# Kernel optimization log

Measured on AMD Instinct MI355X. Metric: run time of the kernel, lower is better.

Reference implementation:

```python
import jax, jax.numpy as jnp
import numpy as np

OUTPUT_SIZE = 16384          # number of map units (must be a perfect square)
SIDE = 128.0                 # sqrt(OUTPUT_SIZE)
SIGMA = 2.0                  # neighbourhood std-dev (non-trainable weight in original)
B, D = 2048, 256


def setup_inputs() -> dict:
    key = jax.random.key(0)
    k1, k2 = jax.random.split(key)
    x = jax.random.normal(k1, (B, D), dtype=jnp.float32)
    kernel = jax.random.normal(k2, (D, OUTPUT_SIZE), dtype=jnp.float32) * 0.1
    return {"x": x, "kernel": kernel}


def _grid_coords():
    # 2D coordinates of each flattened map unit: unit k -> (k // side, k % side)
    idx = jnp.arange(OUTPUT_SIZE, dtype=jnp.float32)
    return jnp.floor(idx / SIDE), jnp.mod(idx, SIDE)  # each (size,)


def reference(x, kernel):
    # Squared Euclidean distance of every sample to every prototype: (B, size).
    # Same math as tf.norm(x[:, :, None] - kernel[None])**2, expressed as a GEMM.
    norms2 = (jnp.sum(x * x, axis=1, keepdims=True)
              - 2.0 * (x @ kernel)
              + jnp.sum(kernel * kernel, axis=0, keepdims=True))
    norms2 = jnp.maximum(norms2, 0.0)

    # Winner-take-all unit per sample, mapped to 2D grid coordinates.
    wta = jnp.argmin(norms2, axis=1).astype(jnp.float32)        # (B,)
    mean_r = jnp.floor(wta / SIDE)                               # (B,)
    mean_c = jnp.mod(wta, SIDE)                                  # (B,)

    # Gaussian neighbourhood over the 2D grid, flattened: (B, size).
    gr, gc = _grid_coords()
    dr = gr[None, :] - mean_r[:, None]
    dc = gc[None, :] - mean_c[:, None]
    radials = jnp.exp(-0.5 / (SIGMA * SIGMA) * (dr * dr + dc * dc))

    return radials * norms2
```

## Files before the change

kernel.cpp:

```cpp
#include <hip/hip_runtime.h>
#include <hip/hip_fp16.h>

#define OUTN 16384
#define BATCH 2048
#define DIM   256

typedef _Float16 half8 __attribute__((ext_vector_type(8)));
typedef float    floatx4 __attribute__((ext_vector_type(4)));
typedef unsigned long long u64;

__device__ __forceinline__ void gl2lds16(const void* g, void* l) {
    __builtin_amdgcn_global_load_lds(
        (const __attribute__((address_space(1))) void*)g,
        (__attribute__((address_space(3))) void*)l, 16, 0, 0);
}

__device__ __forceinline__ u64 packkey(float v, int col) {
    unsigned u = __float_as_uint(v);
    u = (u & 0x80000000u) ? ~u : (u | 0x80000000u);
    return ((u64)u << 32) | (unsigned)col;
}
__device__ __forceinline__ float unpackval(u64 p) {
    unsigned u = (unsigned)(p >> 32);
    u = (u & 0x80000000u) ? (u & 0x7fffffffu) : ~u;
    return __uint_as_float(u);
}

__global__ __launch_bounds__(256) void prep_all(
        const float* __restrict__ x, const float* __restrict__ kern,
        _Float16* __restrict__ xh, float* __restrict__ rown,
        _Float16* __restrict__ kT, float* __restrict__ colnp) {
    int blk = blockIdx.x, t = threadIdx.x;
    if (blk < 512) {
        __shared__ float tile[64][65];
        __shared__ float npart[4][64];
        int tx = t & 63, ty = t >> 6;
        int j0 = (blk >> 1) * 64;
        int dhalf = blk & 1, dbase = dhalf * 128;
        float nrm = 0.f;
        for (int pc = 0; pc < 2; pc++) {
            int dc = dbase + pc * 64;
            __syncthreads();
            for (int it = 0; it < 16; it++) {
                int d = dc + ty + it * 4;
                float v = kern[(size_t)d * OUTN + j0 + tx];
                tile[ty + it * 4][tx] = v;
                nrm = fmaf(v, v, nrm);
            }
            __syncthreads();
            for (int c = t; c < 512; c += 256) {
                int j = c >> 3, o8 = (c & 7) * 8;
                half8 h;
                for (int u = 0; u < 8; u++) h[u] = (_Float16)tile[o8 + u][j];
                *(half8*)&kT[(size_t)(j0 + j) * DIM + dc + o8] = h;
            }
        }
        npart[ty][tx] = nrm;
        __syncthreads();
        if (t < 64)
            colnp[(size_t)dhalf * OUTN + j0 + t] =
                npart[0][t] + npart[1][t] + npart[2][t] + npart[3][t];
    } else {
        int b = blk - 512;
        float v = x[b * DIM + t];
        xh[b * DIM + t] = (_Float16)v;
        float s = v * v;
        for (int off = 32; off; off >>= 1) s += __shfl_down(s, off, 64);
        __shared__ float wsum[4];
        if ((t & 63) == 0) wsum[t >> 6] = s;
        __syncthreads();
        if (t == 0) rown[b] = wsum[0] + wsum[1] + wsum[2] + wsum[3];
    }
}

template <bool NF16>
__global__ __launch_bounds__(256) void gemm_norms(
        const _Float16* __restrict__ xh, const _Float16* __restrict__ kT,
        const float* __restrict__ rown, const float* __restrict__ colnp,
        void* __restrict__ n2out, u64* __restrict__ blockcand) {
    __shared__ __align__(16) char smem[32768];
    _Float16* As = (_Float16*)smem;
    _Float16* Bs = (_Float16*)(smem + 16384);
    u64* cand = (u64*)smem;
    int tid  = threadIdx.x;
    int col0 = blockIdx.x * 128;
    int row0 = blockIdx.y * 128;
    int wid = tid >> 6, lane = tid & 63;
    int wr = wid >> 1, wc = wid & 1;
    int l15 = lane & 15, l4 = lane >> 4;
    int xh7 = l15 & 7;

    floatx4 acc[4][4];
    for (int i = 0; i < 4; i++)
        for (int j = 0; j < 4; j++)
            acc[i][j] = (floatx4){0.f, 0.f, 0.f, 0.f};

    for (int kt = 0; kt < 4; kt++) {
        int k0 = kt * 64;
        for (int it = 0; it < 4; it++) {
            int chunk = it * 256 + tid;
            int r = chunk >> 3, gg = chunk & 7;
            int ksw = (gg ^ (r & 7)) * 8;
            gl2lds16(&xh[(size_t)(row0 + r) * DIM + k0 + ksw], &As[chunk * 8]);
            gl2lds16(&kT[(size_t)(col0 + r) * DIM + k0 + ksw], &Bs[chunk * 8]);
        }
        __syncthreads();
        for (int s = 0; s < 2; s++) {
            int g = s * 4 + l4;
            int sw = (g ^ xh7) * 8;
            half8 af[4], bf[4];
            for (int i = 0; i < 4; i++)
                af[i] = *(half8*)&As[(wr * 64 + i * 16 + l15) * 64 + sw];
            for (int j = 0; j < 4; j++)
                bf[j] = *(half8*)&Bs[(wc * 64 + j * 16 + l15) * 64 + sw];
            for (int i = 0; i < 4; i++)
                for (int j = 0; j < 4; j++)
                    acc[i][j] = __builtin_amdgcn_mfma_f32_16x16x32_f16(
                        af[i], bf[j], acc[i][j], 0, 0, 0);
        }
        __syncthreads();
    }

    float cn[4]; int oc[4];
    for (int j = 0; j < 4; j++) {
        oc[j] = col0 + wc * 64 + j * 16 + l15;
        cn[j] = colnp[oc[j]] + colnp[OUTN + oc[j]];
    }
    for (int i = 0; i < 4; i++) {
        for (int r = 0; r < 4; r++) {
            int row_l = wr * 64 + i * 16 + l4 * 4 + r;
            int orow  = row0 + row_l;
            float rn = rown[orow];
            u64 best = ~0ull;
            for (int j = 0; j < 4; j++) {
                float val = rn + cn[j] - 2.0f * acc[i][j][r];
                size_t oi = (size_t)orow * OUTN + oc[j];
                if (NF16) ((_Float16*)n2out)[oi] = (_Float16)val;
                else      ((float*)n2out)[oi]    = val;
                u64 p = packkey(val, oc[j]);
                if (p < best) best = p;
            }
            cand[row_l * 32 + wc * 16 + l15] = best;
        }
    }
    __syncthreads();
    if (tid < 128) {
        u64 m1 = ~0ull, m2 = ~0ull;
        for (int s = 0; s < 32; s++) {
            u64 v = cand[tid * 32 + s];
            if (v < m1) { m2 = m1; m1 = v; }
            else if (v < m2) { m2 = v; }
        }
        size_t base = (size_t)(row0 + tid) * 256 + blockIdx.x * 2;
        blockcand[base]     = m1;
        blockcand[base + 1] = m2;
    }
}

template <bool NF16>
__global__ __launch_bounds__(256) void refine_finalize(
        const u64* __restrict__ blockcand, const float* __restrict__ x,
        const float* __restrict__ kern, const float* __restrict__ colnp,
        const void* __restrict__ n2in, float* __restrict__ out) {
    int b = blockIdx.x, t = threadIdx.x;
    __shared__ float xrow[DIM];
    __shared__ u64 red[256];
    xrow[t] = x[b * DIM + t];
    u64 e = blockcand[(size_t)b * 256 + t];
    red[t] = e;
    __syncthreads();
    for (int off = 128; off; off >>= 1) {
        if (t < off) { u64 o = red[t + off]; if (o < red[t]) red[t] = o; }
        __syncthreads();
    }
    float minv = unpackval(red[0]);
    __syncthreads();

    float ve = unpackval(e);
    u64 p = ~0ull;
    if (ve <= minv + 0.125f) {
        int j = (int)(e & 0xffffffffu);
        float dot = 0.f;
        for (int d = 0; d < DIM; d++)
            dot = fmaf(xrow[d], kern[(size_t)d * OUTN + j], dot);
        p = packkey((colnp[j] + colnp[OUTN + j]) - 2.0f * dot, j);
    }
    red[t] = p;
    __syncthreads();
    for (int off = 128; off; off >>= 1) {
        if (t < off) { u64 o = red[t + off]; if (o < red[t]) red[t] = o; }
        __syncthreads();
    }
    int w = (int)(red[0] & 0xffffffffu);
    int wrr = w >> 7, wcc = w & 127;

    const _Float16* r16 = (const _Float16*)n2in + (size_t)b * OUTN;
    const float*    r32 = (const float*)n2in    + (size_t)b * OUTN;
    float* rowp = out + (size_t)b * OUTN;
    for (int it = 0; it < 16; it++) {
        int idx4 = it * 256 + t;
        int j0 = idx4 * 4;
        int r  = j0 >> 7, c0 = j0 & 127;
        int dr = r - wrr, drsq = dr * dr;
        float4 res;
        {
            int dc = c0 - wcc;     int d2 = drsq + dc * dc;
            float v = (d2 <= 720) ? (NF16 ? (float)r16[j0]     : r32[j0])     : 0.f;
            res.x = (d2 <= 720) ? __expf(-0.125f * (float)d2) * fmaxf(v, 0.f) : 0.f;
        }
        {
            int dc = c0 + 1 - wcc; int d2 = drsq + dc * dc;
            float v = (d2 <= 720) ? (NF16 ? (float)r16[j0 + 1] : r32[j0 + 1]) : 0.f;
            res.y = (d2 <= 720) ? __expf(-0.125f * (float)d2) * fmaxf(v, 0.f) : 0.f;
        }
        {
            int dc = c0 + 2 - wcc; int d2 = drsq + dc * dc;
            float v = (d2 <= 720) ? (NF16 ? (float)r16[j0 + 2] : r32[j0 + 2]) : 0.f;
            res.z = (d2 <= 720) ? __expf(-0.125f * (float)d2) * fmaxf(v, 0.f) : 0.f;
        }
        {
            int dc = c0 + 3 - wcc; int d2 = drsq + dc * dc;
            float v = (d2 <= 720) ? (NF16 ? (float)r16[j0 + 3] : r32[j0 + 3]) : 0.f;
            res.w = (d2 <= 720) ? __expf(-0.125f * (float)d2) * fmaxf(v, 0.f) : 0.f;
        }
        ((float4*)rowp)[idx4] = res;
    }
}

extern "C" void kernel_launch(void* const* d_in, const int* in_sizes, int n_in,
                              void* d_out, int out_size, void* d_ws, size_t ws_size,
                              hipStream_t stream) {
    const float* x    = (const float*)d_in[0];
    const float* kern = (const float*)d_in[1];
    float* out = (float*)d_out;
    char* ws = (char*)d_ws;

    _Float16* xh   = (_Float16*)(ws);
    _Float16* kT   = (_Float16*)(ws + (1u << 20));
    float*   colnp = (float*)(ws + (9u << 20));
    float*   rown  = (float*)(ws + (9u << 20) + (128u << 10));
    u64* blockcand = (u64*)(ws + (10u << 20));
    void*    n2h   = (void*)(ws + (14u << 20));
    bool f16path = ws_size >= ((size_t)78 << 20);

    prep_all<<<2560, 256, 0, stream>>>(x, kern, xh, rown, kT, colnp);
    if (f16path) {
        gemm_norms<true><<<dim3(OUTN / 128, BATCH / 128), 256, 0, stream>>>(
            xh, kT, rown, colnp, n2h, blockcand);
        refine_finalize<true><<<BATCH, 256, 0, stream>>>(
            blockcand, x, kern, colnp, n2h, out);
    } else {
        gemm_norms<false><<<dim3(OUTN / 128, BATCH / 128), 256, 0, stream>>>(
            xh, kT, rown, colnp, (void*)out, blockcand);
        refine_finalize<false><<<BATCH, 256, 0, stream>>>(
            blockcand, x, kern, colnp, (const void*)out, out);
    }
}
```

Measured before the change: 202.1 us.

## Fuse all stages into one persistent kernel with grid barriers

Replaces the three launches with a single persistent 512-block kernel that uses software grid barriers between the prep, GEMM+candidate, refine and finalize phases. It also adds an fp32 transposed kernel copy so the refine dot product reads contiguously, and stages the fp16 norms tile in LDS for coalesced writes. Finalize now uses separable precomputed Gaussian row/column factors and skips rows beyond the cutoff. The change targets launch overhead and uncoalesced accesses, but it depends on all 512 blocks being co-resident for the spin barrier, drops the fp32 fallback path, and each block serializes four column tiles of GEMM work.

Measured after the change: 502.6 us. 2.49x slower.

```diff
diff --git a/kernel.cpp b/kernel.cpp
--- a/kernel.cpp
+++ b/kernel.cpp
@@ -4,6 +4,7 @@
 #define OUTN 16384
 #define BATCH 2048
 #define DIM   256
+#define NBLK  512
 
 typedef _Float16 half8 __attribute__((ext_vector_type(8)));
 typedef float    floatx4 __attribute__((ext_vector_type(4)));
@@ -26,17 +27,33 @@
     return __uint_as_float(u);
 }
 
-__global__ __launch_bounds__(256) void prep_all(
+__device__ __forceinline__ void gridbar(unsigned* bar, unsigned target) {
+    __syncthreads();
+    __threadfence();
+    if (threadIdx.x == 0) {
+        atomicAdd(bar, 1u);
+        while (atomicAdd(bar, 0u) < target) __builtin_amdgcn_s_sleep(2);
+    }
+    __syncthreads();
+    __threadfence();
+}
+
+__global__ __launch_bounds__(256, 2) void som_fused(
         const float* __restrict__ x, const float* __restrict__ kern,
-        _Float16* __restrict__ xh, float* __restrict__ rown,
-        _Float16* __restrict__ kT, float* __restrict__ colnp) {
-    int blk = blockIdx.x, t = threadIdx.x;
-    if (blk < 512) {
-        __shared__ float tile[64][65];
-        __shared__ float npart[4][64];
+        _Float16* __restrict__ xh, _Float16* __restrict__ kT,
+        float* __restrict__ kT32, float* __restrict__ colnp,
+        float* __restrict__ rown, u64* __restrict__ blockcand,
+        int* __restrict__ wta, _Float16* __restrict__ n2h,
+        float* __restrict__ out, unsigned* __restrict__ bar) {
+    __shared__ __align__(16) char smem[34816];
+    int p = blockIdx.x, t = threadIdx.x;
+
+    {
+        float (*tile)[65] = (float(*)[65])smem;
+        float* npart = (float*)(smem + 16640);
         int tx = t & 63, ty = t >> 6;
-        int j0 = (blk >> 1) * 64;
-        int dhalf = blk & 1, dbase = dhalf * 128;
+        int j0 = (p >> 1) * 64;
+        int dhalf = p & 1, dbase = dhalf * 128;
         float nrm = 0.f;
         for (int pc = 0; pc < 2; pc++) {
             int dc = dbase + pc * 64;
@@ -50,180 +67,194 @@
             __syncthreads();
             for (int c = t; c < 512; c += 256) {
                 int j = c >> 3, o8 = (c & 7) * 8;
-                half8 h;
-                for (int u = 0; u < 8; u++) h[u] = (_Float16)tile[o8 + u][j];
+                half8 h; float vv[8];
+                for (int u = 0; u < 8; u++) { vv[u] = tile[o8 + u][j]; h[u] = (_Float16)vv[u]; }
                 *(half8*)&kT[(size_t)(j0 + j) * DIM + dc + o8] = h;
-            }
-        }
-        npart[ty][tx] = nrm;
+                float* kp = &kT32[(size_t)(j0 + j) * DIM + dc + o8];
+                *(float4*)kp       = make_float4(vv[0], vv[1], vv[2], vv[3]);
+                *(float4*)(kp + 4) = make_float4(vv[4], vv[5], vv[6], vv[7]);
+            }
+        }
+        npart[ty * 64 + tx] = nrm;
         __syncthreads();
         if (t < 64)
             colnp[(size_t)dhalf * OUTN + j0 + t] =
-                npart[0][t] + npart[1][t] + npart[2][t] + npart[3][t];
-    } else {
-        int b = blk - 512;
-        float v = x[b * DIM + t];
-        xh[b * DIM + t] = (_Float16)v;
-        float s = v * v;
-        for (int off = 32; off; off >>= 1) s += __shfl_down(s, off, 64);
-        __shared__ float wsum[4];
-        if ((t & 63) == 0) wsum[t >> 6] = s;
+                npart[t] + npart[64 + t] + npart[128 + t] + npart[192 + t];
         __syncthreads();
-        if (t == 0) rown[b] = wsum[0] + wsum[1] + wsum[2] + wsum[3];
-    }
-}
-
-template <bool NF16>
-__global__ __launch_bounds__(256) void gemm_norms(
-        const _Float16* __restrict__ xh, const _Float16* __restrict__ kT,
-        const float* __restrict__ rown, const float* __restrict__ colnp,
-        void* __restrict__ n2out, u64* __restrict__ blockcand) {
-    __shared__ __align__(16) char smem[32768];
-    _Float16* As = (_Float16*)smem;
-    _Float16* Bs = (_Float16*)(smem + 16384);
-    u64* cand = (u64*)smem;
-    int tid  = threadIdx.x;
-    int col0 = blockIdx.x * 128;
-    int row0 = blockIdx.y * 128;
-    int wid = tid >> 6, lane = tid & 63;
-    int wr = wid >> 1, wc = wid & 1;
-    int l15 = lane & 15, l4 = lane >> 4;
-    int xh7 = l15 & 7;
-
-    floatx4 acc[4][4];
-    for (int i = 0; i < 4; i++)
-        for (int j = 0; j < 4; j++)
-            acc[i][j] = (floatx4){0.f, 0.f, 0.f, 0.f};
-
-    for (int kt = 0; kt < 4; kt++) {
-        int k0 = kt * 64;
-        for (int it = 0; it < 4; it++) {
-            int chunk = it * 256 + tid;
-            int r = chunk >> 3, gg = chunk & 7;
-            int ksw = (gg ^ (r & 7)) * 8;
-            gl2lds16(&xh[(size_t)(row0 + r) * DIM + k0 + ksw], &As[chunk * 8]);
-            gl2lds16(&kT[(size_t)(col0 + r) * DIM + k0 + ksw], &Bs[chunk * 8]);
-        }
-        __syncthreads();
-        for (int s = 0; s < 2; s++) {
-            int g = s * 4 + l4;
-            int sw = (g ^ xh7) * 8;
-            half8 af[4], bf[4];
-            for (int i = 0; i < 4; i++)
-                af[i] = *(half8*)&As[(wr * 64 + i * 16 + l15) * 64 + sw];
-            for (int j = 0; j < 4; j++)
-                bf[j] = *(half8*)&Bs[(wc * 64 + j * 16 + l15) * 64 + sw];
+        for (int q = 0; q < 4; q++) {
+            int b = p * 4 + q;
+            float v = x[b * DIM + t];
+            xh[b * DIM + t] = (_Float16)v;
+            float s = v * v;
+            for (int off = 32; off; off >>= 1) s += __shfl_down(s, off, 64);
+            if ((t & 63) == 0) npart[t >> 6] = s;
+            __syncthreads();
+            if (t == 0) rown[b] = npart[0] + npart[1] + npart[2] + npart[3];
+            __syncthreads();
+        }
+    }
+    gridbar(bar, NBLK);
+
+    {
+        int rb = p >> 5, cg = p & 31;
+        int row0 = rb * 128;
+        int wid = t >> 6, lane = t & 63;
+        int wr = wid >> 1, wc = wid & 1;
+        int l15 = lane & 15, l4 = lane >> 4;
+        int xh7 = l15 & 7;
+        _Float16* As = (_Float16*)smem;
+        _Float16* Bs = (_Float16*)(smem + 16384);
+        u64* cand = (u64*)smem;
+        _Float16* nb = (_Float16*)smem;
+
+        for (int cc = 0; cc < 4; cc++) {
+            int cb = cg * 4 + cc;
+            int col0 = cb * 128;
+            floatx4 acc[4][4];
             for (int i = 0; i < 4; i++)
                 for (int j = 0; j < 4; j++)
-                    acc[i][j] = __builtin_amdgcn_mfma_f32_16x16x32_f16(
-                        af[i], bf[j], acc[i][j], 0, 0, 0);
-        }
+                    acc[i][j] = (floatx4){0.f, 0.f, 0.f, 0.f};
+
+            for (int kt = 0; kt < 4; kt++) {
+                int k0 = kt * 64;
+                for (int it = 0; it < 4; it++) {
+                    int chunk = it * 256 + t;
+                    int r = chunk >> 3, gg = chunk & 7;
+                    int ksw = (gg ^ (r & 7)) * 8;
+                    gl2lds16(&xh[(size_t)(row0 + r) * DIM + k0 + ksw], &As[chunk * 8]);
+                    gl2lds16(&kT[(size_t)(col0 + r) * DIM + k0 + ksw], &Bs[chunk * 8]);
+                }
+                __syncthreads();
+                for (int s = 0; s < 2; s++) {
+                    int g = s * 4 + l4;
+                    int sw = (g ^ xh7) * 8;
+                    half8 af[4], bf[4];
+                    for (int i = 0; i < 4; i++)
+                        af[i] = *(half8*)&As[(wr * 64 + i * 16 + l15) * 64 + sw];
+                    for (int j = 0; j < 4; j++)
+                        bf[j] = *(half8*)&Bs[(wc * 64 + j * 16 + l15) * 64 + sw];
+                    for (int i = 0; i < 4; i++)
+                        for (int j = 0; j < 4; j++)
+                            acc[i][j] = __builtin_amdgcn_mfma_f32_16x16x32_f16(
+                                af[i], bf[j], acc[i][j], 0, 0, 0);
+                }
+                __syncthreads();
+            }
+
+            float cn[4]; int oc[4];
+            for (int j = 0; j < 4; j++) {
+                oc[j] = col0 + wc * 64 + j * 16 + l15;
+                cn[j] = colnp[oc[j]] + colnp[OUTN + oc[j]];
+            }
+            for (int i = 0; i < 4; i++) {
+                for (int r = 0; r < 4; r++) {
+                    int row_l = wr * 64 + i * 16 + l4 * 4 + r;
+                    u64 best = ~0ull;
+                    for (int j = 0; j < 4; j++) {
+                        u64 pk = packkey(cn[j] - 2.0f * acc[i][j][r], oc[j]);
+                        if (pk < best) best = pk;
+                    }
+                    cand[row_l * 33 + wc * 16 + l15] = best;
+                }
+            }
+            __syncthreads();
+            if (t < 128) {
+                u64 m1 = ~0ull, m2 = ~0ull;
+                for (int s = 0; s < 32; s++) {
+                    u64 v = cand[t * 33 + s];
+                    if (v < m1) { m2 = m1; m1 = v; }
+                    else if (v < m2) { m2 = v; }
+                }
+                size_t base = (size_t)(row0 + t) * 256 + cb * 2;
+                blockcand[base]     = m1;
+                blockcand[base + 1] = m2;
+            }
+            __syncthreads();
+            for (int i = 0; i < 4; i++) {
+                for (int r = 0; r < 4; r++) {
+                    int row_l = wr * 64 + i * 16 + l4 * 4 + r;
+                    float rn = rown[row0 + row_l];
+                    for (int j = 0; j < 4; j++)
+                        nb[row_l * 128 + wc * 64 + j * 16 + l15] =
+                            (_Float16)(rn + cn[j] - 2.0f * acc[i][j][r]);
+                }
+            }
+            __syncthreads();
+            for (int c = t; c < 2048; c += 256) {
+                int r = c >> 4, o8 = (c & 15) * 8;
+                *(half8*)&n2h[(size_t)(row0 + r) * OUTN + col0 + o8] =
+                    *(half8*)&nb[r * 128 + o8];
+            }
+            __syncthreads();
+        }
+    }
+    gridbar(bar, 2 * NBLK);
+
+    {
+        float* xrow = (float*)smem;
+        u64*   red  = (u64*)(smem + 1024);
+        for (int q = 0; q < 4; q++) {
+            int b = p * 4 + q;
+            xrow[t] = x[b * DIM + t];
+            u64 e = blockcand[(size_t)b * 256 + t];
+            red[t] = e;
+            __syncthreads();
+            for (int off = 128; off; off >>= 1) {
+                if (t < off) { u64 o = red[t + off]; if (o < red[t]) red[t] = o; }
+                __syncthreads();
+            }
+            float minv = unpackval(red[0]);
+            __syncthreads();
+            u64 pk = ~0ull;
+            if (unpackval(e) <= minv + 0.125f) {
+                int j = (int)(e & 0xffffffffu);
+                const float* kr = kT32 + (size_t)j * DIM;
+                float dot = 0.f;
+                for (int d = 0; d < DIM; d++)
+                    dot = fmaf(xrow[d], kr[d], dot);
+                pk = packkey((colnp[j] + colnp[OUTN + j]) - 2.0f * dot, j);
+            }
+            red[t] = pk;
+            __syncthreads();
+            for (int off = 128; off; off >>= 1) {
+                if (t < off) { u64 o = red[t + off]; if (o < red[t]) red[t] = o; }
+                __syncthreads();
+            }
+            if (t == 0) wta[b] = (int)(red[0] & 0xffffffffu);
+            __syncthreads();
+        }
+    }
+    gridbar(bar, 3 * NBLK);
+
+    {
+        float* colf = (float*)smem;
+        if (t < 128) colf[t] = __expf(-0.125f * (float)(t * t));
         __syncthreads();
-    }
-
-    float cn[4]; int oc[4];
-    for (int j = 0; j < 4; j++) {
-        oc[j] = col0 + wc * 64 + j * 16 + l15;
-        cn[j] = colnp[oc[j]] + colnp[OUTN + oc[j]];
-    }
-    for (int i = 0; i < 4; i++) {
-        for (int r = 0; r < 4; r++) {
-            int row_l = wr * 64 + i * 16 + l4 * 4 + r;
-            int orow  = row0 + row_l;
-            float rn = rown[orow];
-            u64 best = ~0ull;
-            for (int j = 0; j < 4; j++) {
-                float val = rn + cn[j] - 2.0f * acc[i][j][r];
-                size_t oi = (size_t)orow * OUTN + oc[j];
-                if (NF16) ((_Float16*)n2out)[oi] = (_Float16)val;
-                else      ((float*)n2out)[oi]    = val;
-                u64 p = packkey(val, oc[j]);
-                if (p < best) best = p;
-            }
-            cand[row_l * 32 + wc * 16 + l15] = best;
-        }
-    }
-    __syncthreads();
-    if (tid < 128) {
-        u64 m1 = ~0ull, m2 = ~0ull;
-        for (int s = 0; s < 32; s++) {
-            u64 v = cand[tid * 32 + s];
-            if (v < m1) { m2 = m1; m1 = v; }
-            else if (v < m2) { m2 = v; }
-        }
-        size_t base = (size_t)(row0 + tid) * 256 + blockIdx.x * 2;
-        blockcand[base]     = m1;
-        blockcand[base + 1] = m2;
-    }
-}
-
-template <bool NF16>
-__global__ __launch_bounds__(256) void refine_finalize(
-        const u64* __restrict__ blockcand, const float* __restrict__ x,
-        const float* __restrict__ kern, const float* __restrict__ colnp,
-        const void* __restrict__ n2in, float* __restrict__ out) {
-    int b = blockIdx.x, t = threadIdx.x;
-    __shared__ float xrow[DIM];
-    __shared__ u64 red[256];
-    xrow[t] = x[b * DIM + t];
-    u64 e = blockcand[(size_t)b * 256 + t];
-    red[t] = e;
-    __syncthreads();
-    for (int off = 128; off; off >>= 1) {
-        if (t < off) { u64 o = red[t + off]; if (o < red[t]) red[t] = o; }
-        __syncthreads();
-    }
-    float minv = unpackval(red[0]);
-    __syncthreads();
-
-    float ve = unpackval(e);
-    u64 p = ~0ull;
-    if (ve <= minv + 0.125f) {
-        int j = (int)(e & 0xffffffffu);
-        float dot = 0.f;
-        for (int d = 0; d < DIM; d++)
-            dot = fmaf(xrow[d], kern[(size_t)d * OUTN + j], dot);
-        p = packkey((colnp[j] + colnp[OUTN + j]) - 2.0f * dot, j);
-    }
-    red[t] = p;
-    __syncthreads();
-    for (int off = 128; off; off >>= 1) {
-        if (t < off) { u64 o = red[t + off]; if (o < red[t]) red[t] = o; }
-        __syncthreads();
-    }
-    int w = (int)(red[0] & 0xffffffffu);
-    int wrr = w >> 7, wcc = w & 127;
-
-    const _Float16* r16 = (const _Float16*)n2in + (size_t)b * OUTN;
-    const float*    r32 = (const float*)n2in    + (size_t)b * OUTN;
-    float* rowp = out + (size_t)b * OUTN;
-    for (int it = 0; it < 16; it++) {
-        int idx4 = it * 256 + t;
-        int j0 = idx4 * 4;
-        int r  = j0 >> 7, c0 = j0 & 127;
-        int dr = r - wrr, drsq = dr * dr;
-        float4 res;
-        {
-            int dc = c0 - wcc;     int d2 = drsq + dc * dc;
-            float v = (d2 <= 720) ? (NF16 ? (float)r16[j0]     : r32[j0])     : 0.f;
-            res.x = (d2 <= 720) ? __expf(-0.125f * (float)d2) * fmaxf(v, 0.f) : 0.f;
-        }
-        {
-            int dc = c0 + 1 - wcc; int d2 = drsq + dc * dc;
-            float v = (d2 <= 720) ? (NF16 ? (float)r16[j0 + 1] : r32[j0 + 1]) : 0.f;
-            res.y = (d2 <= 720) ? __expf(-0.125f * (float)d2) * fmaxf(v, 0.f) : 0.f;
-        }
-        {
-            int dc = c0 + 2 - wcc; int d2 = drsq + dc * dc;
-            float v = (d2 <= 720) ? (NF16 ? (float)r16[j0 + 2] : r32[j0 + 2]) : 0.f;
-            res.z = (d2 <= 720) ? __expf(-0.125f * (float)d2) * fmaxf(v, 0.f) : 0.f;
-        }
-        {
-            int dc = c0 + 3 - wcc; int d2 = drsq + dc * dc;
-            float v = (d2 <= 720) ? (NF16 ? (float)r16[j0 + 3] : r32[j0 + 3]) : 0.f;
-            res.w = (d2 <= 720) ? __expf(-0.125f * (float)d2) * fmaxf(v, 0.f) : 0.f;
-        }
-        ((float4*)rowp)[idx4] = res;
+        for (int q = 0; q < 4; q++) {
+            int b = p * 4 + q;
+            int w = wta[b];
+            int wrr = w >> 7, wcc = w & 127;
+            const _Float16* nrow = n2h + (size_t)b * OUTN;
+            float* orow = out + (size_t)b * OUTN;
+            for (int c = t; c < 2048; c += 256) {
+                int gr = c >> 4, o8 = (c & 15) * 8;
+                int dr = gr - wrr; if (dr < 0) dr = -dr;
+                float4 r0 = {0.f, 0.f, 0.f, 0.f}, r1 = {0.f, 0.f, 0.f, 0.f};
+                if (dr <= 26) {
+                    float rowf = colf[dr];
+                    half8 h = *(const half8*)&nrow[gr * 128 + o8];
+                    float res[8];
+                    for (int u = 0; u < 8; u++) {
+                        int dc = o8 + u - wcc; if (dc < 0) dc = -dc;
+                        res[u] = rowf * colf[dc] * fmaxf((float)h[u], 0.f);
+                    }
+                    r0 = make_float4(res[0], res[1], res[2], res[3]);
+                    r1 = make_float4(res[4], res[5], res[6], res[7]);
+                }
+                *(float4*)&orow[gr * 128 + o8]     = r0;
+                *(float4*)&orow[gr * 128 + o8 + 4] = r1;
+            }
+        }
     }
 }
 
@@ -237,22 +268,15 @@
 
     _Float16* xh   = (_Float16*)(ws);
     _Float16* kT   = (_Float16*)(ws + (1u << 20));
-    float*   colnp = (float*)(ws + (9u << 20));
-    float*   rown  = (float*)(ws + (9u << 20) + (128u << 10));
-    u64* blockcand = (u64*)(ws + (10u << 20));
-    void*    n2h   = (void*)(ws + (14u << 20));
-    bool f16path = ws_size >= ((size_t)78 << 20);
-
-    prep_all<<<2560, 256, 0, stream>>>(x, kern, xh, rown, kT, colnp);
-    if (f16path) {
-        gemm_norms<true><<<dim3(OUTN / 128, BATCH / 128), 256, 0, stream>>>(
-            xh, kT, rown, colnp, n2h, blockcand);
-        refine_finalize<true><<<BATCH, 256, 0, stream>>>(
-            blockcand, x, kern, colnp, n2h, out);
-    } else {
-        gemm_norms<false><<<dim3(OUTN / 128, BATCH / 128), 256, 0, stream>>>(
-            xh, kT, rown, colnp, (void*)out, blockcand);
-        refine_finalize<false><<<BATCH, 256, 0, stream>>>(
-            blockcand, x, kern, colnp, (const void*)out, out);
-    }
-}
+    float*    kT32 = (float*)(ws + (9u << 20));
+    float*   colnp = (float*)(ws + (25u << 20));
+    float*    rown = (float*)(ws + (25u << 20) + (128u << 10));
+    int*       wta = (int*)(ws + (25u << 20) + (136u << 10));
+    unsigned*  bar = (unsigned*)(ws + (25u << 20) + (144u << 10));
+    u64* blockcand = (u64*)(ws + (26u << 20));
+    _Float16*  n2h = (_Float16*)(ws + (32u << 20));
+
+    hipMemsetAsync(bar, 0, 64, stream);
+    som_fused<<<NBLK, 256, 0, stream>>>(x, kern, xh, kT, kT32, colnp, rown,
+                                        blockcand, wta, n2h, out, bar);
+}
```
